# Performance work log

Measured on AMD Instinct MI355X. Metric: run time of the kernel, lower is better.

## Reference

```python
import jax, jax.numpy as jnp
import numpy as np

NUM_REAL = 19          # real classes (ignore class = index 19 is excluded by cls_counts[:, :-1])
MAX_FEATS_TOTAL = 10000
TEMPERATURE = 0.5
EPS_NORM = 1e-12       # torch F.normalize eps


def setup_inputs() -> dict:
    key = jax.random.key(0)
    k1, k2 = jax.random.split(key)
    label = jax.random.randint(k1, (4, 1024, 1024), 0, NUM_REAL, dtype=jnp.int32)
    features = jax.random.normal(k2, (4, 256, 256, 256), dtype=jnp.float32)
    return {"label": label, "features": features}


def _forward(label, features):
    n, c, fh, fw = features.shape
    scale = label.shape[-1] // fw
    # get_dist_and_classes: nearest-neighbour downsample == strided slice (exact divisor)
    dom = label[:, ::scale, ::scale].reshape(n, -1)               # [N, P]
    P = dom.shape[1]
    feats = features.reshape(n, c, P)                             # [N, C, P]

    # sample_anchors_fast: all NUM_REAL classes present in every image (guaranteed by setup),
    # so total_cls and views_per_class are static (the max_features_total cap path).
    T = n * NUM_REAL
    V = MAX_FEATS_TOTAL // T

    mask = dom[:, None, :] == jnp.arange(NUM_REAL, dtype=dom.dtype)[None, :, None]  # [N,K,P]
    pix = jnp.arange(P, dtype=jnp.int32)
    # key > 0 iff pixel belongs to class; larger key = earlier pixel -> top_k picks the
    # first V member pixels per (image, class) (deterministic stand-in for randperm)
    sel_key = jnp.where(mask, P - pix, -pix)
    _, idx = jax.lax.top_k(sel_key, V)                            # [N, K, V]

    sampled = jnp.take_along_axis(feats[:, None, :, :], idx[:, :, None, :], axis=3)  # [N,K,C,V]
    sampled = sampled.reshape(T, c, V)                            # batch-major, class ascending
    labels = jnp.tile(jnp.arange(NUM_REAL, dtype=jnp.float32), n) # [T]

    # contrastive_loss
    norm = jnp.sqrt(jnp.sum(sampled * sampled, axis=1, keepdims=True))
    f = sampled / jnp.maximum(norm, EPS_NORM)                     # L2 normalize over C
    f = jnp.transpose(f, (0, 2, 1)).reshape(T * V, c)             # [T*V, C]
    lab = jnp.repeat(labels, V)                                   # [T*V]

    eq = (lab[:, None] == lab[None, :]).astype(f.dtype)           # [TV, TV]
    M = T * V
    d = jnp.arange(M)
    pos_mask = eq.at[d, d].set(0.0)

    logits = (f @ f.T) / TEMPERATURE
    exp_l = jnp.exp(logits)                                       # original has no max-subtraction
    neg_sum = jnp.sum(exp_l * (1.0 - eq), axis=1, keepdims=True)
    log_prob = logits - jnp.log(exp_l + neg_sum)
    mean_log_prob_pos = jnp.sum(pos_mask * log_prob, axis=1) / jnp.sum(pos_mask, axis=1)
    return -jnp.mean(mean_log_prob_pos)


def reference(label, features):
    return _forward(label, features)
```

## Files before the change

### kernel.cpp

```cpp
#include <hip/hip_runtime.h>
#include <hip/hip_bf16.h>

#define NUM_REAL 19
#define NIMG     4
#define T_TOT    76
#define V_SEL    131
#define M_ROWS   9956
#define MP       9984
#define CDIM     256
#define P_PIX    65536
#define TILE     128
#define BK       32
#define RPI      2489
#define NT1      3081
#define NCHUNK   32
#define CHPIX    2048
#define CT       5
#define NT2      (NUM_REAL * 15)

typedef __attribute__((ext_vector_type(8))) short short8;
typedef __attribute__((ext_vector_type(4))) float floatx4;

__device__ __forceinline__ void gld_lds16(const unsigned short* g, unsigned short* l) {
    __builtin_amdgcn_global_load_lds((__attribute__((address_space(1))) void*)(g),
                                     (__attribute__((address_space(3))) void*)(l),
                                     16, 0, 0);
}

__global__ __launch_bounds__(256) void k_hist(const int* __restrict__ label,
                                              int* __restrict__ ghist)
{
    __shared__ int h[NUM_REAL];
    const int img = blockIdx.y, ch = blockIdx.x, tid = threadIdx.x;
    if (tid < NUM_REAL) h[tid] = 0;
    __syncthreads();
    const int* lab = label + img * 1048576;
    const int p0 = ch * CHPIX + tid * 8;
    #pragma unroll
    for (int j = 0; j < 8; ++j) {
        int p = p0 + j;
        int c = lab[((p >> 8) << 12) + ((p & 255) << 2)];
        atomicAdd(&h[c], 1);
    }
    __syncthreads();
    if (tid < NUM_REAL) ghist[(img * NCHUNK + ch) * NUM_REAL + tid] = h[tid];
}

__global__ __launch_bounds__(256) void k_scatter(const int* __restrict__ label,
                                                 const int* __restrict__ ghist,
                                                 int* __restrict__ sel)
{
    __shared__ int cnt[NUM_REAL * 256];
    const int img = blockIdx.y, ch = blockIdx.x, tid = threadIdx.x;
    #pragma unroll
    for (int k = 0; k < NUM_REAL; ++k) cnt[k * 256 + tid] = 0;
    __shared__ int base[NUM_REAL];
    if (tid < NUM_REAL) {
        int b = 0;
        for (int q = 0; q < ch; ++q) b += ghist[(img * NCHUNK + q) * NUM_REAL + tid];
        base[tid] = b;
    }
    const int* lab = label + img * 1048576;
    const int p0 = ch * CHPIX + tid * 8;
    #pragma unroll
    for (int j = 0; j < 8; ++j) {
        int p = p0 + j;
        int c = lab[((p >> 8) << 12) + ((p & 255) << 2)];
        cnt[c * 256 + tid]++;
    }
    __syncthreads();
    if (tid < NUM_REAL) {
        int run = base[tid], bb = tid * 256;
        for (int t2 = 0; t2 < 256; ++t2) {
            int tmp = cnt[bb + t2];
            cnt[bb + t2] = run;
            run += tmp;
        }
    }
    __syncthreads();
    bool need = false;
    #pragma unroll
    for (int k = 0; k < NUM_REAL; ++k) if (cnt[k * 256 + tid] < V_SEL) need = true;
    if (need) {
        for (int j = 0; j < 8; ++j) {
            int p = p0 + j;
            int c = lab[((p >> 8) << 12) + ((p & 255) << 2)];
            int r = cnt[c * 256 + tid]++;
            if (r < V_SEL) sel[(img * NUM_REAL + c) * V_SEL + r] = p;
        }
    }
}

__global__ __launch_bounds__(256) void k_gather1(const float* __restrict__ feats,
                                                 const int* __restrict__ sel,
                                                 float* __restrict__ Ftmp,
                                                 float* __restrict__ nrm)
{
    __shared__ int pbuf[RPI];
    const int b  = blockIdx.y;
    const int c0 = blockIdx.x * 4;
    const int tid = threadIdx.x;
    for (int s = tid; s < RPI; s += 256) pbuf[s] = sel[b * RPI + s];
    __syncthreads();
    const float* f0 = feats + (size_t)(b * CDIM + c0) * P_PIX;
    for (int r = tid; r < RPI; r += 256) {
        int p = pbuf[r];
        float x0 = f0[p];
        float x1 = f0[p + P_PIX];
        float x2 = f0[p + 2 * P_PIX];
        float x3 = f0[p + 3 * P_PIX];
        int row = b * RPI + r;
        float4 v = make_float4(x0, x1, x2, x3);
        *reinterpret_cast<float4*>(Ftmp + (size_t)row * CDIM + c0) = v;
        atomicAdd(&nrm[row], x0 * x0 + x1 * x1 + x2 * x2 + x3 * x3);
    }
}

__global__ __launch_bounds__(256) void k_gather2(const float* __restrict__ Ftmp,
                                                 const float* __restrict__ nrm,
                                                 unsigned short* __restrict__ F)
{
    const int row = blockIdx.x * 4 + (threadIdx.x >> 6);
    const int c4  = (threadIdx.x & 63) * 4;
    ushort4 o;
    if (row < M_ROWS) {
        float4 v = *reinterpret_cast<const float4*>(Ftmp + (size_t)row * CDIM + c4);
        float rinv = 1.0f / fmaxf(sqrtf(nrm[row]), 1e-12f);
        __hip_bfloat16 h0 = __float2bfloat16(v.x * rinv);
        __hip_bfloat16 h1 = __float2bfloat16(v.y * rinv);
        __hip_bfloat16 h2 = __float2bfloat16(v.z * rinv);
        __hip_bfloat16 h3 = __float2bfloat16(v.w * rinv);
        o.x = *reinterpret_cast<unsigned short*>(&h0);
        o.y = *reinterpret_cast<unsigned short*>(&h1);
        o.z = *reinterpret_cast<unsigned short*>(&h2);
        o.w = *reinterpret_cast<unsigned short*>(&h3);
    } else {
        o.x = o.y = o.z = o.w = 0;
    }
    *reinterpret_cast<ushort4*>(F + (size_t)row * CDIM + c4) = o;
}

__global__ __launch_bounds__(256) void k_gemm(const unsigned short* __restrict__ F,
                                              float* __restrict__ negsum)
{
    __shared__ unsigned short As[2][TILE * BK];
    __shared__ unsigned short Bs[2][TILE * BK];

    int t = blockIdx.x;
    int bi = (int)((157.0f - sqrtf(24649.0f - 8.0f * (float)t)) * 0.5f);
    if (bi < 0) bi = 0;
    if (bi > 77) bi = 77;
    while ((bi + 1) * 78 - ((bi + 1) * bi) / 2 <= t) ++bi;
    while (bi * 78 - (bi * (bi - 1)) / 2 > t) --bi;
    int bj = bi + (t - (bi * 78 - (bi * (bi - 1)) / 2));
    const bool diag = (bi == bj);
    const int i0 = bi * TILE, j0 = bj * TILE;

    const int tid  = threadIdx.x;
    const int wave = tid >> 6, lane = tid & 63;
    const int qr = lane >> 4, lr = lane & 15;
    const int wr = (wave >> 1) * 64, wc = (wave & 1) * 64;

    floatx4 acc[4][4];
    floatx4 zero4 = {0.f, 0.f, 0.f, 0.f};
    #pragma unroll
    for (int a = 0; a < 4; ++a)
        #pragma unroll
        for (int b = 0; b < 4; ++b) acc[a][b] = zero4;

    const int srow = wave * 32 + (lane >> 2);
    const int scol = (lane & 3) * 8;
    const unsigned short* gA = F + (size_t)(i0 + srow) * CDIM + scol;
    const unsigned short* gB = F + (size_t)(j0 + srow) * CDIM + scol;
    const int l0 = (wave * 32) * BK, l1 = (wave * 32 + 16) * BK;

    gld_lds16(gA,             &As[0][l0]);
    gld_lds16(gA + 16 * CDIM, &As[0][l1]);
    gld_lds16(gB,             &Bs[0][l0]);
    gld_lds16(gB + 16 * CDIM, &Bs[0][l1]);

    #pragma unroll 2
    for (int k = 0; k < 8; ++k) {
        __syncthreads();
        const int cur = k & 1, nxt = cur ^ 1;
        if (k < 7) {
            const int kc = (k + 1) * BK;
            gld_lds16(gA + kc,             &As[nxt][l0]);
            gld_lds16(gA + kc + 16 * CDIM, &As[nxt][l1]);
            gld_lds16(gB + kc,             &Bs[nxt][l0]);
            gld_lds16(gB + kc + 16 * CDIM, &Bs[nxt][l1]);
        }
        short8 a[4], b[4];
        #pragma unroll
        for (int mi = 0; mi < 4; ++mi)
            a[mi] = *reinterpret_cast<const short8*>(&As[cur][(wr + mi * 16 + lr) * BK + qr * 8]);
        #pragma unroll
        for (int ni = 0; ni < 4; ++ni)
            b[ni] = *reinterpret_cast<const short8*>(&Bs[cur][(wc + ni * 16 + lr) * BK + qr * 8]);
        #pragma unroll
        for (int mi = 0; mi < 4; ++mi)
            #pragma unroll
            for (int ni = 0; ni < 4; ++ni)
                acc[mi][ni] = __builtin_amdgcn_mfma_f32_16x16x32_bf16(a[mi], b[ni], acc[mi][ni], 0, 0, 0);
    }

    int jcls[4];
    bool jval[4];
    #pragma unroll
    for (int ni = 0; ni < 4; ++ni) {
        int gcol = j0 + wc + ni * 16 + lr;
        jval[ni] = gcol < M_ROWS;
        unsigned tj = (unsigned)gcol / V_SEL;
        jcls[ni] = (int)(tj - (tj / NUM_REAL) * NUM_REAL);
    }
    float* red  = (float*)&As[0][0];
    float* cred = (float*)&Bs[0][0];
    float colacc[4] = {0.f, 0.f, 0.f, 0.f};
    #pragma unroll
    for (int mi = 0; mi < 4; ++mi) {
        #pragma unroll
        for (int reg = 0; reg < 4; ++reg) {
            int rloc = wr + mi * 16 + qr * 4 + reg;
            int grow = i0 + rloc;
            bool ival = grow < M_ROWS;
            unsigned ti = (unsigned)grow / V_SEL;
            int icls = (int)(ti - (ti / NUM_REAL) * NUM_REAL);
            float rowacc = 0.f;
            #pragma unroll
            for (int ni = 0; ni < 4; ++ni) {
                bool v = ival && jval[ni] && (icls != jcls[ni]);
                float e = v ? __expf(acc[mi][ni][reg] * 2.0f) : 0.f;
                rowacc += e;
                colacc[ni] += e;
            }
            rowacc += __shfl_xor(rowacc, 1, 64);
            rowacc += __shfl_xor(rowacc, 2, 64);
            rowacc += __shfl_xor(rowacc, 4, 64);
            rowacc += __shfl_xor(rowacc, 8, 64);
            if (lr == 0) red[rloc * 2 + (wave & 1)] = rowacc;
        }
    }
    #pragma unroll
    for (int ni = 0; ni < 4; ++ni) {
        float cc = colacc[ni];
        cc += __shfl_xor(cc, 16, 64);
        cc += __shfl_xor(cc, 32, 64);
        if (qr == 0) cred[(wc + ni * 16 + lr) * 2 + (wave >> 1)] = cc;
    }
    __syncthreads();
    if (tid < 128) {
        int row = i0 + tid;
        if (row < M_ROWS) atomicAdd(&negsum[row], red[tid * 2] + red[tid * 2 + 1]);
    } else {
        int cc2 = tid - 128, col = j0 + cc2;
        if (!diag && col < M_ROWS) atomicAdd(&negsum[col], cred[cc2 * 2] + cred[cc2 * 2 + 1]);
    }
}

__global__ __launch_bounds__(256) void k_pos(const unsigned short* __restrict__ F,
                                             const float* __restrict__ negsum,
                                             float* __restrict__ out)
{
    __shared__ unsigned short As[2][TILE * BK];
    __shared__ unsigned short Bs[2][TILE * BK];
    __shared__ float wred[4];

    const int c = blockIdx.x / 15;
    int pidx = blockIdx.x % 15;
    int ti = 0;
    while (pidx >= CT - ti) { pidx -= CT - ti; ++ti; }
    const int tj = ti + pidx;
    const int u0i = ti * TILE, u0j = tj * TILE;
    const bool offd = (ti != tj);

    const int tid  = threadIdx.x;
    const int wave = tid >> 6, lane = tid & 63;
    const int qr = lane >> 4, lr = lane & 15;
    const int wr = (wave >> 1) * 64, wc = (wave & 1) * 64;

    floatx4 acc[4][4];
    floatx4 zero4 = {0.f, 0.f, 0.f, 0.f};
    #pragma unroll
    for (int a = 0; a < 4; ++a)
        #pragma unroll
        for (int b = 0; b < 4; ++b) acc[a][b] = zero4;

    const int srow = wave * 32 + (lane >> 2);
    const int scol = (lane & 3) * 8;
    auto growmap = [&](int u) -> int {
        int uc = u < 524 ? u : 523;
        int b = uc / 131, v = uc - 131 * b;
        return b * RPI + c * V_SEL + v;
    };
    const unsigned short* gA0 = F + (size_t)growmap(u0i + srow) * CDIM + scol;
    const unsigned short* gA1 = F + (size_t)growmap(u0i + srow + 16) * CDIM + scol;
    const unsigned short* gB0 = F + (size_t)growmap(u0j + srow) * CDIM + scol;
    const unsigned short* gB1 = F + (size_t)growmap(u0j + srow + 16) * CDIM + scol;
    const int l0 = (wave * 32) * BK, l1 = (wave * 32 + 16) * BK;

    gld_lds16(gA0, &As[0][l0]);
    gld_lds16(gA1, &As[0][l1]);
    gld_lds16(gB0, &Bs[0][l0]);
    gld_lds16(gB1, &Bs[0][l1]);

    #pragma unroll 2
    for (int k = 0; k < 8; ++k) {
        __syncthreads();
        const int cur = k & 1, nxt = cur ^ 1;
        if (k < 7) {
            const int kc = (k + 1) * BK;
            gld_lds16(gA0 + kc, &As[nxt][l0]);
            gld_lds16(gA1 + kc, &As[nxt][l1]);
            gld_lds16(gB0 + kc, &Bs[nxt][l0]);
            gld_lds16(gB1 + kc, &Bs[nxt][l1]);
        }
        short8 a[4], b[4];
        #pragma unroll
        for (int mi = 0; mi < 4; ++mi)
            a[mi] = *reinterpret_cast<const short8*>(&As[cur][(wr + mi * 16 + lr) * BK + qr * 8]);
        #pragma unroll
        for (int ni = 0; ni < 4; ++ni)
            b[ni] = *reinterpret_cast<const short8*>(&Bs[cur][(wc + ni * 16 + lr) * BK + qr * 8]);
        #pragma unroll
        for (int mi = 0; mi < 4; ++mi)
            #pragma unroll
            for (int ni = 0; ni < 4; ++ni)
                acc[mi][ni] = __builtin_amdgcn_mfma_f32_16x16x32_bf16(a[mi], b[ni], acc[mi][ni], 0, 0, 0);
    }

    int  ujv[4];
    bool jval[4];
    float nsj[4];
    #pragma unroll
    for (int ni = 0; ni < 4; ++ni) {
        int uj = u0j + wc + ni * 16 + lr;
        ujv[ni] = uj;
        jval[ni] = uj < 524;
        nsj[ni] = jval[ni] ? negsum[growmap(uj)] : 0.f;
    }
    float tsum = 0.f;
    #pragma unroll
    for (int mi = 0; mi < 4; ++mi) {
        #pragma unroll
        for (int reg = 0; reg < 4; ++reg) {
            int ui = u0i + wr + mi * 16 + qr * 4 + reg;
            bool ival = ui < 524;
            float nsi = ival ? negsum[growmap(ui)] : 0.f;
            #pragma unroll
            for (int ni = 0; ni < 4; ++ni) {
                if (ival && jval[ni] && ui != ujv[ni]) {
                    float l  = acc[mi][ni][reg] * 2.0f;
                    float el = __expf(l);
                    tsum += l - __logf(el + nsi);
                    if (offd) tsum += l - __logf(el + nsj[ni]);
                }
            }
        }
    }
    #pragma unroll
    for (int s = 32; s > 0; s >>= 1) tsum += __shfl_xor(tsum, s, 64);
    if (lane == 0) wred[wave] = tsum;
    __syncthreads();
    if (tid == 0) {
        const float scale = -1.0f / (523.0f * (float)M_ROWS);
        atomicAdd(out, (wred[0] + wred[1] + wred[2] + wred[3]) * scale);
    }
}

extern "C" void kernel_launch(void* const* d_in, const int* in_sizes, int n_in,
                              void* d_out, int out_size, void* d_ws, size_t ws_size,
                              hipStream_t stream)
{
    const int*   label = (const int*)d_in[0];
    const float* feats = (const float*)d_in[1];
    float*       out   = (float*)d_out;

    char* ws = (char*)d_ws;
    unsigned short* F = (unsigned short*)ws;
    size_t off = (size_t)MP * CDIM * 2;
    int* sel = (int*)(ws + off);
    off += (size_t)T_TOT * V_SEL * 4;
    off = (off + 255) & ~(size_t)255;
    float* negsum = (float*)(ws + off);
    off += (size_t)MP * 4;
    float* nrm = (float*)(ws + off);
    off += (size_t)MP * 4;
    int* ghist = (int*)(ws + off);
    off += (size_t)NIMG * NCHUNK * NUM_REAL * 4;
    off = (off + 255) & ~(size_t)255;
    float* Ftmp = (float*)(ws + off);

    hipMemsetAsync(negsum, 0, (size_t)MP * 8, stream);
    hipMemsetAsync(out, 0, sizeof(float), stream);

    dim3 gh(NCHUNK, NIMG);
    k_hist<<<gh, 256, 0, stream>>>(label, ghist);
    k_scatter<<<gh, 256, 0, stream>>>(label, ghist, sel);
    dim3 g1(CDIM / 4, NIMG);
    k_gather1<<<g1, 256, 0, stream>>>(feats, sel, Ftmp, nrm);
    k_gather2<<<MP / 4, 256, 0, stream>>>(Ftmp, nrm, F);
    k_gemm<<<NT1, 256, 0, stream>>>(F, negsum);
    k_pos<<<NT2, 256, 0, stream>>>(F, negsum, out);
}
```

Before: 432.2 us.

## Fuse gather and normalization into one kernel, fold memsets, parallelize scan

Replaces the two-pass gather (an fp32 temp buffer plus atomic norm accumulation, then a separate normalize-to-bf16 pass) with a single kernel in which one wavefront gathers a row's 256 channels, reduces the norm with shuffles and writes bf16 directly. The two memsets move into the histogram kernel, and the serial per-class prefix scan in the scatter kernel becomes a wave-level shuffle scan. This removes the temp buffer traffic, the atomics and three launches. In exchange, each lane's gather loads are strided by P_PIX across channels, so a wave's loads hit 64 separate cache lines where neighbouring lanes previously read neighbouring rows.

```diff
diff --git a/kernel.cpp b/kernel.cpp
--- a/kernel.cpp
+++ b/kernel.cpp
@@ -28,10 +28,19 @@
 }
 
 __global__ __launch_bounds__(256) void k_hist(const int* __restrict__ label,
-                                              int* __restrict__ ghist)
+                                              int* __restrict__ ghist,
+                                              float* __restrict__ negsum,
+                                              float* __restrict__ out)
 {
     __shared__ int h[NUM_REAL];
     const int img = blockIdx.y, ch = blockIdx.x, tid = threadIdx.x;
+    if (img == 0) {
+        #pragma unroll
+        for (int i = 0; i < (MP / NCHUNK); i += 256)
+            if (i + tid < (MP / NCHUNK))
+                negsum[ch * (MP / NCHUNK) + i + tid] = 0.f;
+        if (ch == 0 && tid == 0) out[0] = 0.f;
+    }
     if (tid < NUM_REAL) h[tid] = 0;
     __syncthreads();
     const int* lab = label + img * 1048576;
@@ -51,10 +60,10 @@
                                                  int* __restrict__ sel)
 {
     __shared__ int cnt[NUM_REAL * 256];
+    __shared__ int base[NUM_REAL];
     const int img = blockIdx.y, ch = blockIdx.x, tid = threadIdx.x;
     #pragma unroll
     for (int k = 0; k < NUM_REAL; ++k) cnt[k * 256 + tid] = 0;
-    __shared__ int base[NUM_REAL];
     if (tid < NUM_REAL) {
         int b = 0;
         for (int q = 0; q < ch; ++q) b += ghist[(img * NCHUNK + q) * NUM_REAL + tid];
@@ -69,13 +78,26 @@
         cnt[c * 256 + tid]++;
     }
     __syncthreads();
-    if (tid < NUM_REAL) {
-        int run = base[tid], bb = tid * 256;
-        for (int t2 = 0; t2 < 256; ++t2) {
-            int tmp = cnt[bb + t2];
-            cnt[bb + t2] = run;
-            run += tmp;
-        }
+    const int wave = tid >> 6, lane = tid & 63;
+    for (int k = wave; k < NUM_REAL; k += 4) {
+        const int bb = k * 256;
+        int x0 = cnt[bb + lane],       x1 = cnt[bb + 64 + lane],
+            x2 = cnt[bb + 128 + lane], x3 = cnt[bb + 192 + lane];
+        const int v0 = x0, v1 = x1, v2 = x2, v3 = x3;
+        #pragma unroll
+        for (int d = 1; d < 64; d <<= 1) {
+            int t0 = __shfl_up(x0, d, 64), t1 = __shfl_up(x1, d, 64);
+            int t2 = __shfl_up(x2, d, 64), t3 = __shfl_up(x3, d, 64);
+            if (lane >= d) { x0 += t0; x1 += t1; x2 += t2; x3 += t3; }
+        }
+        const int s0 = __shfl(x0, 63, 64);
+        const int s1 = __shfl(x1, 63, 64);
+        const int s2 = __shfl(x2, 63, 64);
+        const int b0 = base[k];
+        cnt[bb + lane]       = b0 + x0 - v0;
+        cnt[bb + 64 + lane]  = b0 + s0 + x1 - v1;
+        cnt[bb + 128 + lane] = b0 + s0 + s1 + x2 - v2;
+        cnt[bb + 192 + lane] = b0 + s0 + s1 + s2 + x3 - v3;
     }
     __syncthreads();
     bool need = false;
@@ -91,53 +113,39 @@
     }
 }
 
-__global__ __launch_bounds__(256) void k_gather1(const float* __restrict__ feats,
-                                                 const int* __restrict__ sel,
-                                                 float* __restrict__ Ftmp,
-                                                 float* __restrict__ nrm)
-{
-    __shared__ int pbuf[RPI];
-    const int b  = blockIdx.y;
-    const int c0 = blockIdx.x * 4;
-    const int tid = threadIdx.x;
-    for (int s = tid; s < RPI; s += 256) pbuf[s] = sel[b * RPI + s];
-    __syncthreads();
-    const float* f0 = feats + (size_t)(b * CDIM + c0) * P_PIX;
-    for (int r = tid; r < RPI; r += 256) {
-        int p = pbuf[r];
-        float x0 = f0[p];
-        float x1 = f0[p + P_PIX];
-        float x2 = f0[p + 2 * P_PIX];
-        float x3 = f0[p + 3 * P_PIX];
-        int row = b * RPI + r;
-        float4 v = make_float4(x0, x1, x2, x3);
-        *reinterpret_cast<float4*>(Ftmp + (size_t)row * CDIM + c0) = v;
-        atomicAdd(&nrm[row], x0 * x0 + x1 * x1 + x2 * x2 + x3 * x3);
-    }
-}
-
-__global__ __launch_bounds__(256) void k_gather2(const float* __restrict__ Ftmp,
-                                                 const float* __restrict__ nrm,
-                                                 unsigned short* __restrict__ F)
-{
-    const int row = blockIdx.x * 4 + (threadIdx.x >> 6);
-    const int c4  = (threadIdx.x & 63) * 4;
-    ushort4 o;
-    if (row < M_ROWS) {
-        float4 v = *reinterpret_cast<const float4*>(Ftmp + (size_t)row * CDIM + c4);
-        float rinv = 1.0f / fmaxf(sqrtf(nrm[row]), 1e-12f);
-        __hip_bfloat16 h0 = __float2bfloat16(v.x * rinv);
-        __hip_bfloat16 h1 = __float2bfloat16(v.y * rinv);
-        __hip_bfloat16 h2 = __float2bfloat16(v.z * rinv);
-        __hip_bfloat16 h3 = __float2bfloat16(v.w * rinv);
-        o.x = *reinterpret_cast<unsigned short*>(&h0);
-        o.y = *reinterpret_cast<unsigned short*>(&h1);
-        o.z = *reinterpret_cast<unsigned short*>(&h2);
-        o.w = *reinterpret_cast<unsigned short*>(&h3);
-    } else {
-        o.x = o.y = o.z = o.w = 0;
-    }
-    *reinterpret_cast<ushort4*>(F + (size_t)row * CDIM + c4) = o;
+__global__ __launch_bounds__(256) void k_gather(const float* __restrict__ feats,
+                                                const int* __restrict__ sel,
+                                                unsigned short* __restrict__ F)
+{
+    __shared__ unsigned short rowbuf[4][256];
+    const int tid = threadIdx.x, wave = tid >> 6, lane = tid & 63;
+    const int r = blockIdx.x * 4 + wave;
+    if (r < M_ROWS) {
+        const int b = r / RPI;
+        const int p = sel[r];
+        const float* f0 = feats + (size_t)b * CDIM * P_PIX + p;
+        float x0 = f0[(size_t)(lane      ) * P_PIX];
+        float x1 = f0[(size_t)(lane + 64 ) * P_PIX];
+        float x2 = f0[(size_t)(lane + 128) * P_PIX];
+        float x3 = f0[(size_t)(lane + 192) * P_PIX];
+        float ss = x0 * x0 + x1 * x1 + x2 * x2 + x3 * x3;
+        #pragma unroll
+        for (int d = 1; d < 64; d <<= 1) ss += __shfl_xor(ss, d, 64);
+        const float rinv = 1.0f / fmaxf(sqrtf(ss), 1e-12f);
+        __hip_bfloat16 h0 = __float2bfloat16(x0 * rinv);
+        __hip_bfloat16 h1 = __float2bfloat16(x1 * rinv);
+        __hip_bfloat16 h2 = __float2bfloat16(x2 * rinv);
+        __hip_bfloat16 h3 = __float2bfloat16(x3 * rinv);
+        rowbuf[wave][lane      ] = *reinterpret_cast<unsigned short*>(&h0);
+        rowbuf[wave][lane + 64 ] = *reinterpret_cast<unsigned short*>(&h1);
+        rowbuf[wave][lane + 128] = *reinterpret_cast<unsigned short*>(&h2);
+        rowbuf[wave][lane + 192] = *reinterpret_cast<unsigned short*>(&h3);
+        ushort4 o = *reinterpret_cast<ushort4*>(&rowbuf[wave][lane * 4]);
+        *reinterpret_cast<ushort4*>(F + (size_t)r * CDIM + lane * 4) = o;
+    } else if (r < MP) {
+        ushort4 z; z.x = z.y = z.z = z.w = 0;
+        *reinterpret_cast<ushort4*>(F + (size_t)r * CDIM + lane * 4) = z;
+    }
 }
 
 __global__ __launch_bounds__(256) void k_gemm(const unsigned short* __restrict__ F,
@@ -383,22 +391,13 @@
     off = (off + 255) & ~(size_t)255;
     float* negsum = (float*)(ws + off);
     off += (size_t)MP * 4;
-    float* nrm = (float*)(ws + off);
-    off += (size_t)MP * 4;
     int* ghist = (int*)(ws + off);
     off += (size_t)NIMG * NCHUNK * NUM_REAL * 4;
-    off = (off + 255) & ~(size_t)255;
-    float* Ftmp = (float*)(ws + off);
-
-    hipMemsetAsync(negsum, 0, (size_t)MP * 8, stream);
-    hipMemsetAsync(out, 0, sizeof(float), stream);
 
     dim3 gh(NCHUNK, NIMG);
-    k_hist<<<gh, 256, 0, stream>>>(label, ghist);
+    k_hist<<<gh, 256, 0, stream>>>(label, ghist, negsum, out);
     k_scatter<<<gh, 256, 0, stream>>>(label, ghist, sel);
-    dim3 g1(CDIM / 4, NIMG);
-    k_gather1<<<g1, 256, 0, stream>>>(feats, sel, Ftmp, nrm);
-    k_gather2<<<MP / 4, 256, 0, stream>>>(Ftmp, nrm, F);
+    k_gather<<<MP / 4, 256, 0, stream>>>(feats, sel, F);
     k_gemm<<<NT1, 256, 0, stream>>>(F, negsum);
     k_pos<<<NT2, 256, 0, stream>>>(F, negsum, out);
 }
```

After: 418.2 us. -3.2%, faster.
